# Optimization experiments

Hardware: AMD Instinct MI355X
Metric: run time of the kernel (lower is better)

## Reference

```python
import jax, jax.numpy as jnp
import numpy as np


def _h(s):
    # Step function: 0 where s > 0, else 1 (zero gradient everywhere).
    return jnp.where(s > 0, 0.0, 1.0).astype(s.dtype)


def setup_inputs() -> dict:
    key = jax.random.key(0)
    k1, k2, k3 = jax.random.split(key, 3)
    B, T = 4096, 2048
    x = jax.random.normal(k1, (B, T, 1), dtype=jnp.float32)
    out_prev = jax.random.normal(k2, (B, 1, 1), dtype=jnp.float32)
    lstm_outs = jax.random.normal(k3, (B, T, 4), dtype=jnp.float32)
    return {"x": x, "out_prev": out_prev, "lstm_outs": lstm_outs}


def reference(x, out_prev, lstm_outs):
    # x: [B, T, 1], out_prev: [B, 1, 1] (only first step used), lstm_outs: [B, T, 4]
    xT = jnp.swapaxes(x, 0, 1)          # [T, B, 1]
    wT = jnp.swapaxes(lstm_outs, 0, 1)  # [T, B, 4]

    def step(prev, inputs):
        # prev: [B, 1]
        xt, wt = inputs                  # [B, 1], [B, 4]
        m_lo = wt[:, 0:1]
        m_up = wt[:, 1:2]
        c_lo = wt[:, 2:3]
        c_up = wt[:, 3:4]
        # h() arguments use detached weights in the original (grad is zero through
        # the step function anyway); stop_gradient kept for faithfulness.
        m_lo_d = jax.lax.stop_gradient(m_lo)
        m_up_d = jax.lax.stop_gradient(m_up)
        c_lo_d = jax.lax.stop_gradient(c_lo)
        c_up_d = jax.lax.stop_gradient(c_up)
        f1 = _h((m_lo_d * xt + m_lo_d * c_lo_d - prev) / m_lo_d)
        f2 = _h((prev - m_up_d * xt - m_up_d * c_up_d) / m_up_d)
        out = (m_lo * xt * f1 + m_lo * c_lo * f1
               + m_up * xt * f2 + m_up * c_up * f2
               + prev * (1.0 - f1) * (1.0 - f2))
        return out, out

    init = out_prev[:, 0, :]             # [B, 1]
    _, outs = jax.lax.scan(step, init, (xT, wT))  # outs: [T, B, 1]
    custom_output = jnp.swapaxes(outs, 0, 1)      # [B, T, 1]
    # Original also returns (lstm_outs, 0, 0, 0) passthrough; main output is below.
    return custom_output
```

## Files before the change

### kernel.cpp

```cpp
#include <hip/hip_runtime.h>


#define C 32
#define NCH 64

#define WG_BARRIER() asm volatile("s_waitcnt lgkmcnt(0)\ns_barrier" ::: "memory")

__global__ __launch_bounds__(192) void pc_scan(
    const float* __restrict__ x, const float* __restrict__ p0,
    const float4* __restrict__ lstm4, float* __restrict__ out,
    int B, int T) {
#pragma clang fp contract(off)
  __shared__ float4 tileA[2][C * 17];
  __shared__ float4 tileB[2][C * 17];
  __shared__ float ostg[2][16 * 36];

  const int tid = threadIdx.x;
  const int b0 = blockIdx.x * 16;
  const float4* x4 = reinterpret_cast<const float4*>(x);
  float4* out4 = reinterpret_cast<float4*>(out);

  const int q = tid - 64;
  const int pj = (q >> 3) & 15;
  const int pk = q & 7;

  float4 X0, X1, L00, L01, L02, L03, L10, L11, L12, L13;

#define ISSUE(S, CH)                                              \
  if (tid >= 64) {                                                \
    size_t base = (size_t)(b0 + pj) * T + (CH) * C + 4 * pk;      \
    X##S = x4[base >> 2];                                         \
    L##S##0 = lstm4[base + 0];                                    \
    L##S##1 = lstm4[base + 1];                                    \
    L##S##2 = lstm4[base + 2];                                    \
    L##S##3 = lstm4[base + 3];                                    \
  }

#define STAGE_ELT(S, I, XC, BUF)                                            \
  {                                                                         \
    float4 wv = L##S##I;                                                    \
    float xv = XC;                                                          \
    float a1 = wv.x * xv, a2 = wv.x * wv.z;                                 \
    float L1v = a1 + a2;                                                    \
    unsigned s1m = __float_as_uint(wv.x) & 0x80000000u;                     \
    float L1f = __uint_as_float(__float_as_uint(L1v) ^ s1m);                \
    float a3 = wv.y * xv, a4 = wv.y * wv.w;                                 \
    unsigned f2m = (__float_as_uint(wv.y) & 0x80000000u) ^ 0x80000000u;     \
    float a3f = __uint_as_float(__float_as_uint(a3) ^ f2m);                 \
    float a4f = __uint_as_float(__float_as_uint(a4) ^ f2m);                 \
    float V01 = a3 + a4;                                                    \
    float V11 = (L1v + a3) + a4;                                            \
    int s = 4 * pk + I;                                                     \
    tileA[BUF][s * 17 + pj] =                                               \
        make_float4(__uint_as_float(s1m), L1f, __uint_as_float(f2m), a3f);  \
    tileB[BUF][s * 17 + pj] = make_float4(a4f, V11, V01, L1v);              \
  }

#define STAGE(S, BUF)                    \
  if (tid >= 64) {                       \
    STAGE_ELT(S, 0, X##S.x, BUF)         \
    STAGE_ELT(S, 1, X##S.y, BUF)         \
    STAGE_ELT(S, 2, X##S.z, BUF)         \
    STAGE_ELT(S, 3, X##S.w, BUF)         \
  }

#define FLUSH(CP, BP)                                                       \
  if (tid >= 64) {                                                          \
    float4 v = *(const float4*)&ostg[BP][pj * 36 + 4 * pk];                 \
    out4[((size_t)(b0 + pj) * T + (CP) * C + 4 * pk) >> 2] = v;             \
  }

#define SCAN(BUF)                                                           \
  if (tid < 16) {                                                           \
    _Pragma("unroll") for (int s = 0; s < C; ++s) {                         \
      float4 A = tileA[BUF][s * 17 + tid];                                  \
      float4 Bv = tileB[BUF][s * 17 + tid];                                 \
      unsigned pu = __float_as_uint(p);                                     \
      float pf = __uint_as_float(pu ^ __float_as_uint(A.x));                \
      bool c1 = pf >= A.y;                                                  \
      float pp = __uint_as_float(pu ^ __float_as_uint(A.z));                \
      float qv = pp - A.w;                                                  \
      bool c2 = qv >= Bv.x;                                                 \
      float i1 = c1 ? Bv.y : Bv.z;                                          \
      float i2 = c1 ? Bv.w : p;                                             \
      p = c2 ? i1 : i2;                                                     \
      ostg[BUF][tid * 36 + s] = p;                                          \
    }                                                                       \
  }

  float p = (tid < 16) ? p0[b0 + tid] : 0.0f;

  ISSUE(0, 0)
  STAGE(0, 0)
  ISSUE(1, 1)
  WG_BARRIER();

  for (int c = 0; c < NCH; c += 2) {
    if (c + 2 < NCH) ISSUE(0, c + 2)
    STAGE(1, 1)
    if (c >= 1) FLUSH(c - 1, 1)
    SCAN(0)
    WG_BARRIER();

    if (c + 3 < NCH) ISSUE(1, c + 3)
    if (c + 2 < NCH) STAGE(0, 0)
    FLUSH(c, 0)
    SCAN(1)
    WG_BARRIER();
  }
  FLUSH(NCH - 1, 1)
}

extern "C" void kernel_launch(void* const* d_in, const int* in_sizes, int n_in,
                              void* d_out, int out_size, void* d_ws, size_t ws_size,
                              hipStream_t stream) {
  const float* x = (const float*)d_in[0];
  const float* op = (const float*)d_in[1];
  const float4* lstm = (const float4*)d_in[2];
  int B = in_sizes[1];
  int T = in_sizes[0] / B;
  hipLaunchKernelGGL(pc_scan, dim3(B / 16), dim3(192), 0, stream,
                     x, op, lstm, (float*)d_out, B, T);
}
```

Measured before the change: 260.4 us.

## Double scan chunk length and restage tiles row-major per batch with x via LDS

Raises the per-chunk time span from 32 to 64 steps, which halves the number of chunks and therefore the workgroup barriers and pipeline handoffs per row. The LDS tiles switch to a per-batch-row layout with padded strides. x is now staged through a shared buffer, and each loader thread fetches eight strided float4s instead of four contiguous ones. The trade-off is higher register pressure from holding 16 prefetched float4s plus x, a larger LDS footprint, and a longer serial scan between barriers.

Result: faster. 237.4 us (-8.8%).

```diff
diff --git a/kernel.cpp b/kernel.cpp
--- a/kernel.cpp
+++ b/kernel.cpp
@@ -1,8 +1,10 @@
 #include <hip/hip_runtime.h>
 
 
-#define C 32
-#define NCH 64
+#define C 64
+#define NCH 32
+#define TS 65
+#define XS 68
 
 #define WG_BARRIER() asm volatile("s_waitcnt lgkmcnt(0)\ns_barrier" ::: "memory")
 
@@ -11,9 +13,10 @@
     const float4* __restrict__ lstm4, float* __restrict__ out,
     int B, int T) {
 #pragma clang fp contract(off)
-  __shared__ float4 tileA[2][C * 17];
-  __shared__ float4 tileB[2][C * 17];
-  __shared__ float ostg[2][16 * 36];
+  __shared__ float4 tileA[2][16 * TS];
+  __shared__ float4 tileB[2][16 * TS];
+  __shared__ float xt[16 * XS];
+  __shared__ float ostg[2][16 * XS];
 
   const int tid = threadIdx.x;
   const int b0 = blockIdx.x * 16;
@@ -24,68 +27,79 @@
   const int pj = (q >> 3) & 15;
   const int pk = q & 7;
 
-  float4 X0, X1, L00, L01, L02, L03, L10, L11, L12, L13;
+  float4 L00, L01, L02, L03, L04, L05, L06, L07;
+  float4 L10, L11, L12, L13, L14, L15, L16, L17;
+  float4 X00, X01, X10, X11;
 
-#define ISSUE(S, CH)                                              \
-  if (tid >= 64) {                                                \
-    size_t base = (size_t)(b0 + pj) * T + (CH) * C + 4 * pk;      \
-    X##S = x4[base >> 2];                                         \
-    L##S##0 = lstm4[base + 0];                                    \
-    L##S##1 = lstm4[base + 1];                                    \
-    L##S##2 = lstm4[base + 2];                                    \
-    L##S##3 = lstm4[base + 3];                                    \
+#define ISSUE(S, CH)                                                    \
+  if (tid >= 64) {                                                      \
+    size_t rb = (size_t)(b0 + pj) * T + (size_t)(CH) * C;               \
+    const float4* lp = lstm4 + rb + pk;                                 \
+    L##S##0 = lp[0];  L##S##1 = lp[8];  L##S##2 = lp[16];               \
+    L##S##3 = lp[24]; L##S##4 = lp[32]; L##S##5 = lp[40];               \
+    L##S##6 = lp[48]; L##S##7 = lp[56];                                 \
+    X##S##0 = x4[(rb >> 2) + 2 * pk];                                   \
+    X##S##1 = x4[(rb >> 2) + 2 * pk + 1];                               \
   }
 
-#define STAGE_ELT(S, I, XC, BUF)                                            \
-  {                                                                         \
-    float4 wv = L##S##I;                                                    \
-    float xv = XC;                                                          \
-    float a1 = wv.x * xv, a2 = wv.x * wv.z;                                 \
-    float L1v = a1 + a2;                                                    \
-    unsigned s1m = __float_as_uint(wv.x) & 0x80000000u;                     \
-    float L1f = __uint_as_float(__float_as_uint(L1v) ^ s1m);                \
-    float a3 = wv.y * xv, a4 = wv.y * wv.w;                                 \
-    unsigned f2m = (__float_as_uint(wv.y) & 0x80000000u) ^ 0x80000000u;     \
-    float a3f = __uint_as_float(__float_as_uint(a3) ^ f2m);                 \
-    float a4f = __uint_as_float(__float_as_uint(a4) ^ f2m);                 \
-    float V01 = a3 + a4;                                                    \
-    float V11 = (L1v + a3) + a4;                                            \
-    int s = 4 * pk + I;                                                     \
-    tileA[BUF][s * 17 + pj] =                                               \
-        make_float4(__uint_as_float(s1m), L1f, __uint_as_float(f2m), a3f);  \
-    tileB[BUF][s * 17 + pj] = make_float4(a4f, V11, V01, L1v);              \
+#define STAGE_ELT(LV, SS, BUF)                                          \
+  {                                                                     \
+    float4 wv = LV;                       \
+    float xv = xt[pj * XS + (SS)];                                      \
+    float a1 = wv.x * xv, a2 = wv.x * wv.z;                             \
+    float L1v = a1 + a2;                                                \
+    unsigned s1m = __float_as_uint(wv.x) & 0x80000000u;                 \
+    float L1f = __uint_as_float(__float_as_uint(L1v) ^ s1m);            \
+    float a3 = wv.y * xv, a4 = wv.y * wv.w;                             \
+    unsigned f2m = (__float_as_uint(wv.y) & 0x80000000u) ^ 0x80000000u; \
+    float a3f = __uint_as_float(__float_as_uint(a3) ^ f2m);             \
+    float a4f = __uint_as_float(__float_as_uint(a4) ^ f2m);             \
+    float V01 = a3 + a4;                                                \
+    float V11 = (L1v + a3) + a4;                                        \
+    tileA[BUF][pj * TS + (SS)] =                                        \
+        make_float4(__uint_as_float(s1m), L1f, __uint_as_float(f2m), a3f); \
+    tileB[BUF][pj * TS + (SS)] = make_float4(a4f, V11, V01, L1v);       \
   }
 
-#define STAGE(S, BUF)                    \
-  if (tid >= 64) {                       \
-    STAGE_ELT(S, 0, X##S.x, BUF)         \
-    STAGE_ELT(S, 1, X##S.y, BUF)         \
-    STAGE_ELT(S, 2, X##S.z, BUF)         \
-    STAGE_ELT(S, 3, X##S.w, BUF)         \
+#define STAGE(S, BUF)                                                   \
+  if (tid >= 64) {                                                      \
+    *(float4*)&xt[pj * XS + 8 * pk] = X##S##0;                          \
+    *(float4*)&xt[pj * XS + 8 * pk + 4] = X##S##1;                      \
+    STAGE_ELT(L##S##0, pk,      BUF)                                    \
+    STAGE_ELT(L##S##1, pk + 8,  BUF)                                    \
+    STAGE_ELT(L##S##2, pk + 16, BUF)                                    \
+    STAGE_ELT(L##S##3, pk + 24, BUF)                                    \
+    STAGE_ELT(L##S##4, pk + 32, BUF)                                    \
+    STAGE_ELT(L##S##5, pk + 40, BUF)                                    \
+    STAGE_ELT(L##S##6, pk + 48, BUF)                                    \
+    STAGE_ELT(L##S##7, pk + 56, BUF)                                    \
   }
 
-#define FLUSH(CP, BP)                                                       \
-  if (tid >= 64) {                                                          \
-    float4 v = *(const float4*)&ostg[BP][pj * 36 + 4 * pk];                 \
-    out4[((size_t)(b0 + pj) * T + (CP) * C + 4 * pk) >> 2] = v;             \
+#define FLUSH(CP, OB)                                                   \
+  if (tid >= 64) {                                                      \
+    float4 v0 = *(const float4*)&ostg[OB][pj * XS + 8 * pk];            \
+    float4 v1 = *(const float4*)&ostg[OB][pj * XS + 8 * pk + 4];        \
+    size_t ob = ((size_t)(b0 + pj) * T + (size_t)(CP) * C) >> 2;        \
+    out4[ob + 2 * pk] = v0;                                             \
+    out4[ob + 2 * pk + 1] = v1;                                         \
   }
 
-#define SCAN(BUF)                                                           \
-  if (tid < 16) {                                                           \
-    _Pragma("unroll") for (int s = 0; s < C; ++s) {                         \
-      float4 A = tileA[BUF][s * 17 + tid];                                  \
-      float4 Bv = tileB[BUF][s * 17 + tid];                                 \
-      unsigned pu = __float_as_uint(p);                                     \
-      float pf = __uint_as_float(pu ^ __float_as_uint(A.x));                \
-      bool c1 = pf >= A.y;                                                  \
-      float pp = __uint_as_float(pu ^ __float_as_uint(A.z));                \
-      float qv = pp - A.w;                                                  \
-      bool c2 = qv >= Bv.x;                                                 \
-      float i1 = c1 ? Bv.y : Bv.z;                                          \
-      float i2 = c1 ? Bv.w : p;                                             \
-      p = c2 ? i1 : i2;                                                     \
-      ostg[BUF][tid * 36 + s] = p;                                          \
-    }                                                                       \
+#define SCAN(BUF, OB)                                                   \
+  if (tid < 16) {                                                       \
+    _Pragma("unroll") for (int s = 0; s < C; ++s) {                     \
+      float4 A = tileA[BUF][tid * TS + s];                              \
+      float4 Bv = tileB[BUF][tid * TS + s];                             \
+      unsigned pu = __float_as_uint(p);                                 \
+      float pf = __uint_as_float(pu ^ __float_as_uint(A.x));            \
+      bool c1 = pf >= A.y;                                              \
+      float pp = __uint_as_float(pu ^ __float_as_uint(A.z));            \
+      float qv = pp - A.w;                                              \
+      bool c2 = qv >= Bv.x;                                             \
+      float i1 = c1 ? Bv.y : Bv.z;                                      \
+      float i2 = c1 ? Bv.w : p;                                         \
+      p = c2 ? i1 : i2;                                                 \
+      ostg[OB][tid * XS + s] = p;                                       \
+    }                                                                   \
   }
 
   float p = (tid < 16) ? p0[b0 + tid] : 0.0f;
@@ -99,13 +113,13 @@
     if (c + 2 < NCH) ISSUE(0, c + 2)
     STAGE(1, 1)
     if (c >= 1) FLUSH(c - 1, 1)
-    SCAN(0)
+    SCAN(0, 0)
     WG_BARRIER();
 
     if (c + 3 < NCH) ISSUE(1, c + 3)
     if (c + 2 < NCH) STAGE(0, 0)
     FLUSH(c, 0)
-    SCAN(1)
+    SCAN(1, 1)
     WG_BARRIER();
   }
   FLUSH(NCH - 1, 1)
```
